# Optimization experiments

Measured on AMD Instinct MI355X. Metric: run time of the kernel, lower is better.

Reference implementation:

```python
import jax, jax.numpy as jnp
import numpy as np

N, E, IN, HID, OUT, H = 10000, 320000, 256, 128, 128, 4
SLOPE = 0.2

def setup_inputs() -> dict:
    key = jax.random.key(0)
    ks = jax.random.split(key, 12)
    s = lambda d: 1.0 / np.sqrt(d)
    return {
        "x": jax.random.normal(ks[0], (N, IN), jnp.float32),
        "edge_index": jax.random.randint(ks[1], (2, E), 0, N, jnp.int32),
        "W1": jax.random.normal(ks[2], (IN, H * HID), jnp.float32) * s(IN),
        "a_src1": jax.random.normal(ks[3], (H, HID), jnp.float32) * s(HID),
        "a_dst1": jax.random.normal(ks[4], (H, HID), jnp.float32) * s(HID),
        "b1": jnp.zeros((H * HID,), jnp.float32),
        "W2": jax.random.normal(ks[5], (H * HID, H * OUT), jnp.float32) * s(H * HID),
        "a_src2": jax.random.normal(ks[6], (H, OUT), jnp.float32) * s(OUT),
        "a_dst2": jax.random.normal(ks[7], (H, OUT), jnp.float32) * s(OUT),
        "b2": jnp.zeros((OUT,), jnp.float32),
    }

def _gat_layer(x, src, dst, W, a_src, a_dst, bias, concat, C):
    n = x.shape[0]
    h = (x @ W).reshape(n, H, C)                      # [N,H,C]
    alpha_s = jnp.einsum('nhc,hc->nh', h, a_src)      # [N,H]
    alpha_d = jnp.einsum('nhc,hc->nh', h, a_dst)
    e = jax.nn.leaky_relu(alpha_s[src] + alpha_d[dst], SLOPE)  # [E,H]
    # segment softmax over incoming edges of each dst node
    m = jax.ops.segment_max(e, dst, num_segments=n)   # [N,H]
    m = jnp.where(jnp.isfinite(m), m, 0.0)
    ex = jnp.exp(e - m[dst])
    denom = jax.ops.segment_sum(ex, dst, num_segments=n)
    alpha = ex / (denom[dst] + 1e-16)                 # [E,H]
    msg = h[src] * alpha[:, :, None]                  # [E,H,C]
    out = jax.ops.segment_sum(msg, dst, num_segments=n)  # [N,H,C]
    out = out.reshape(n, H * C) if concat else out.mean(axis=1)
    return out + bias

def reference(x, edge_index, W1, a_src1, a_dst1, b1, W2, a_src2, a_dst2, b2):
    n = x.shape[0]
    loops = jnp.arange(n, dtype=edge_index.dtype)
    src = jnp.concatenate([edge_index[0], loops])
    dst = jnp.concatenate([edge_index[1], loops])
    h = _gat_layer(x, src, dst, W1, a_src1, a_dst1, b1, True, HID)
    h = jax.nn.relu(h)  # dropout is identity in eval mode
    out = _gat_layer(h, src, dst, W2, a_src2, a_dst2, b2, False, OUT)
    return out
```

## Files before the change

### kernel.cpp

```cpp
#include <hip/hip_runtime.h>
#include <hip/hip_fp16.h>
#include <math.h>

#define Nn 10000
#define Ee 320000
#define EE 330000
#define INF_ 256
#define NH 4
#define OUTC 128
#define F1 512
#define F2 512
#define SLOPE 0.2f
#define STRIDE 80

#define SC_BLOCKS 1290
#define CONVX_BLOCKS 2500
#define TW1_BLOCKS 512
#define TW2_BLOCKS 1024

static __device__ __forceinline__ float lrelu(float x) { return fmaxf(x, SLOPE * x); }

using frag_ab = __attribute__((ext_vector_type(8))) _Float16;
using frag_c  = __attribute__((ext_vector_type(4))) float;

__global__ void prep(const int* __restrict__ ei, int* counts, int* __restrict__ csr,
                     const float* __restrict__ x, const float* __restrict__ W1,
                     const float* __restrict__ W2, _Float16* __restrict__ xh,
                     _Float16* __restrict__ w1t, _Float16* __restrict__ w2t) {
    int b = blockIdx.x, t = threadIdx.x;
    if (b < SC_BLOCKS) {
        int e = b * 256 + t;
        if (e < EE) {
            int src, dst;
            if (e < Ee) { src = ei[e]; dst = ei[Ee + e]; }
            else        { src = e - Ee; dst = e - Ee; }
            int slot = atomicAdd(&counts[dst], 1);
            if (slot < STRIDE) csr[dst * STRIDE + slot] = src;
        }
    } else if (b < SC_BLOCKS + CONVX_BLOCKS) {
        int i = ((b - SC_BLOCKS) * 256 + t) * 4;
        float4 v = *(const float4*)(x + i);
        _Float16 oh[4];
        oh[0] = (_Float16)v.x; oh[1] = (_Float16)v.y;
        oh[2] = (_Float16)v.z; oh[3] = (_Float16)v.w;
        *(float2*)(xh + i) = *(float2*)oh;
    } else if (b < SC_BLOCKS + CONVX_BLOCKS + TW1_BLOCKS) {
        int bb = b - SC_BLOCKS - CONVX_BLOCKS;
        int n = (bb & 7) * 64 + (t & 63);
        int k = (bb >> 3) * 4 + (t >> 6);
        w1t[(size_t)n * INF_ + k] = (_Float16)W1[(size_t)k * F1 + n];
    } else {
        int bb = b - SC_BLOCKS - CONVX_BLOCKS - TW1_BLOCKS;
        int n = (bb & 7) * 64 + (t & 63);
        int k = (bb >> 3) * 4 + (t >> 6);
        w2t[(size_t)n * F1 + k] = (_Float16)W2[(size_t)k * F2 + n];
    }
}

#define LDK 40
__global__ __launch_bounds__(256) void mfma_gemm(const _Float16* __restrict__ A,
                                                 const _Float16* __restrict__ BT,
                                                 _Float16* __restrict__ C,
                                                 const float* __restrict__ a_src,
                                                 const float* __restrict__ a_dst,
                                                 float* __restrict__ as_out,
                                                 float* __restrict__ ad_out,
                                                 int M, int K) {
    __shared__ _Float16 As[64 * LDK];
    __shared__ _Float16 Bs[128 * LDK];
    const int tid = threadIdx.x;
    const int wave = tid >> 6, lane = tid & 63;
    const int q = lane >> 4, ml = lane & 15;
    const int bm = blockIdx.x * 64, bn = blockIdx.y * 128;
    const int head = blockIdx.y;
    const int srow = tid >> 2, scol = (tid & 3) * 8;

    frag_c acc[8];
#pragma unroll
    for (int f = 0; f < 8; f++)
#pragma unroll
        for (int r = 0; r < 4; r++) acc[f][r] = 0.f;

    for (int k0 = 0; k0 < K; k0 += 32) {
        int gm = bm + srow;
        frag_ab av;
        if (gm < M) av = *(const frag_ab*)(A + (size_t)gm * K + k0 + scol);
        else {
#pragma unroll
            for (int j = 0; j < 8; j++) av[j] = (_Float16)0.f;
        }
        *(frag_ab*)&As[srow * LDK + scol] = av;
        *(frag_ab*)&Bs[srow * LDK + scol] =
            *(const frag_ab*)(BT + (size_t)(bn + srow) * K + k0 + scol);
        *(frag_ab*)&Bs[(64 + srow) * LDK + scol] =
            *(const frag_ab*)(BT + (size_t)(bn + 64 + srow) * K + k0 + scol);
        __syncthreads();
        frag_ab a = *(frag_ab*)&As[(wave * 16 + ml) * LDK + q * 8];
#pragma unroll
        for (int f = 0; f < 8; f++) {
            frag_ab b = *(frag_ab*)&Bs[(f * 16 + ml) * LDK + q * 8];
            acc[f] = __builtin_amdgcn_mfma_f32_16x16x32_f16(a, b, acc[f], 0, 0, 0);
        }
        __syncthreads();
    }
    float asum[4] = {}, dsum[4] = {};
#pragma unroll
    for (int f = 0; f < 8; f++) {
        int cl = f * 16 + ml;
        int col = bn + cl;
        float sa = a_src[head * 128 + cl];
        float da = a_dst[head * 128 + cl];
#pragma unroll
        for (int r = 0; r < 4; r++) {
            int row = bm + wave * 16 + q * 4 + r;
            if (row < M) C[(size_t)row * (NH * 128) + col] = (_Float16)acc[f][r];
            asum[r] += acc[f][r] * sa;
            dsum[r] += acc[f][r] * da;
        }
    }
#pragma unroll
    for (int r = 0; r < 4; r++) {
#pragma unroll
        for (int off = 1; off < 16; off <<= 1) {
            asum[r] += __shfl_xor(asum[r], off);
            dsum[r] += __shfl_xor(dsum[r], off);
        }
    }
    if (ml == 0) {
#pragma unroll
        for (int r = 0; r < 4; r++) {
            int row = bm + wave * 16 + q * 4 + r;
            if (row < M) {
                as_out[(size_t)head * M + row] = asum[r];
                ad_out[(size_t)head * M + row] = dsum[r];
            }
        }
    }
}

__global__ __launch_bounds__(256) void passAB1(const int* __restrict__ counts,
                                               const int* __restrict__ csr,
                                               const float* __restrict__ as,
                                               const float* __restrict__ ad,
                                               const _Float16* __restrict__ hh,
                                               const float* __restrict__ b1,
                                               _Float16* __restrict__ agg) {
    __shared__ int2 ew[16][84];
    int head = blockIdx.x & 3;
    int qw = threadIdx.x >> 4;
    int l = threadIdx.x & 15;
    int n = (blockIdx.x >> 2) * 16 + qw;
    int deg = counts[n]; if (deg > STRIDE) deg = STRIDE;
    int pdeg = (deg + 7) & ~7;
    const float* ash = as + (size_t)head * Nn;
    float adh = ad[(size_t)head * Nn + n];
    int base = n * STRIDE;
    float m = -1e30f;
    for (int k = l; k < pdeg; k += 16) {
        int src = 0; float v = -1e30f;
        if (k < deg) {
            src = csr[base + k];
            v = lrelu(ash[src] + adh);
        }
        ew[qw][k] = make_int2(src, __float_as_int(v));
        m = fmaxf(m, v);
    }
    m = fmaxf(m, __shfl_xor(m, 1));
    m = fmaxf(m, __shfl_xor(m, 2));
    m = fmaxf(m, __shfl_xor(m, 4));
    m = fmaxf(m, __shfl_xor(m, 8));
    float s = 0.f;
    for (int k = l; k < pdeg; k += 16) {
        float e = __expf(__int_as_float(ew[qw][k].y) - m);
        ew[qw][k].y = __float_as_int(e);
        s += e;
    }
    s += __shfl_xor(s, 1);
    s += __shfl_xor(s, 2);
    s += __shfl_xor(s, 4);
    s += __shfl_xor(s, 8);
    float inv = 1.f / (s + 1e-16f);
    int c = head * 128 + (l << 3);
    float acc[8] = {};
    for (int kk = 0; kk < pdeg; kk += 8) {
        int2 p[8];
#pragma unroll
        for (int j = 0; j < 8; j++) p[j] = ew[qw][kk + j];
#pragma unroll
        for (int j = 0; j < 8; j++) {
            float w = __int_as_float(p[j].y);
            frag_ab r = *(const frag_ab*)(hh + (size_t)p[j].x * F1 + c);
#pragma unroll
            for (int u = 0; u < 8; u++) acc[u] = fmaf((float)r[u], w, acc[u]);
        }
    }
    _Float16 oh[8];
#pragma unroll
    for (int j = 0; j < 8; j++)
        oh[j] = (_Float16)fmaxf(acc[j] * inv + b1[c + j], 0.f);
    *(float4*)&agg[(size_t)n * F1 + c] = *(float4*)oh;
}

__global__ __launch_bounds__(256) void passAB2(const int* __restrict__ counts,
                                               const int* __restrict__ csr,
                                               const float* __restrict__ as,
                                               const float* __restrict__ ad,
                                               const _Float16* __restrict__ hh,
                                               _Float16* __restrict__ tmp) {
    __shared__ int2 ew[16][84];
    int head = blockIdx.x & 3;
    int qw = threadIdx.x >> 4;
    int l = threadIdx.x & 15;
    int n = (blockIdx.x >> 2) * 16 + qw;
    int deg = counts[n]; if (deg > STRIDE) deg = STRIDE;
    int pdeg = (deg + 7) & ~7;
    const float* ash = as + (size_t)head * Nn;
    float adh = ad[(size_t)head * Nn + n];
    int base = n * STRIDE;
    float m = -1e30f;
    for (int k = l; k < pdeg; k += 16) {
        int src = 0; float v = -1e30f;
        if (k < deg) {
            src = csr[base + k];
            v = lrelu(ash[src] + adh);
        }
        ew[qw][k] = make_int2(src, __float_as_int(v));
        m = fmaxf(m, v);
    }
    m = fmaxf(m, __shfl_xor(m, 1));
    m = fmaxf(m, __shfl_xor(m, 2));
    m = fmaxf(m, __shfl_xor(m, 4));
    m = fmaxf(m, __shfl_xor(m, 8));
    float s = 0.f;
    for (int k = l; k < pdeg; k += 16) {
        float e = __expf(__int_as_float(ew[qw][k].y) - m);
        ew[qw][k].y = __float_as_int(e);
        s += e;
    }
    s += __shfl_xor(s, 1);
    s += __shfl_xor(s, 2);
    s += __shfl_xor(s, 4);
    s += __shfl_xor(s, 8);
    float inv = 1.f / (s + 1e-16f);
    int c = head * 128 + (l << 3);
    float acc[8] = {};
    for (int kk = 0; kk < pdeg; kk += 8) {
        int2 p[8];
#pragma unroll
        for (int j = 0; j < 8; j++) p[j] = ew[qw][kk + j];
#pragma unroll
        for (int j = 0; j < 8; j++) {
            float w = __int_as_float(p[j].y);
            frag_ab r = *(const frag_ab*)(hh + (size_t)p[j].x * F2 + c);
#pragma unroll
            for (int u = 0; u < 8; u++) acc[u] = fmaf((float)r[u], w, acc[u]);
        }
    }
    float qq = 0.25f * inv;
    _Float16 oh[8];
#pragma unroll
    for (int j = 0; j < 8; j++) oh[j] = (_Float16)(acc[j] * qq);
    *(float4*)&tmp[(size_t)n * F2 + c] = *(float4*)oh;
}

__global__ void reduce4(const _Float16* __restrict__ tmp, const float* __restrict__ b2,
                        float* __restrict__ out) {
    int i = blockIdx.x * 256 + threadIdx.x;
    if (i >= Nn * OUTC) return;
    int n = i >> 7, oc = i & 127;
    const _Float16* tp = tmp + (size_t)n * 512 + oc;
    out[i] = (float)tp[0] + (float)tp[128] + (float)tp[256] + (float)tp[384] + b2[oc];
}

extern "C" void kernel_launch(void* const* d_in, const int* in_sizes, int n_in,
                              void* d_out, int out_size, void* d_ws, size_t ws_size,
                              hipStream_t stream) {
    const float* x      = (const float*)d_in[0];
    const int*   ei     = (const int*)d_in[1];
    const float* W1     = (const float*)d_in[2];
    const float* a_src1 = (const float*)d_in[3];
    const float* a_dst1 = (const float*)d_in[4];
    const float* b1     = (const float*)d_in[5];
    const float* W2     = (const float*)d_in[6];
    const float* a_src2 = (const float*)d_in[7];
    const float* a_dst2 = (const float*)d_in[8];
    const float* b2     = (const float*)d_in[9];
    float* out = (float*)d_out;

    const size_t NF = (size_t)Nn * F1;
    float* f = (float*)d_ws;
    _Float16* tmp = (_Float16*)f;
    float* as1   = f + NF;
    float* ad1   = as1 + Nn;
    float* as1h  = as1;
    float* ad1h  = as1 + (size_t)NH * Nn;
    float* as2h  = ad1h + (size_t)NH * Nn;
    float* ad2h  = as2h + (size_t)NH * Nn;
    (void)ad1;
    int* csr     = (int*)(ad2h + (size_t)NH * Nn);
    _Float16* hh   = (_Float16*)(csr + (size_t)Nn * STRIDE);
    _Float16* aggh = hh + NF;
    _Float16* xh   = aggh + NF;
    _Float16* w1t  = xh + (size_t)Nn * INF_;
    _Float16* w2t  = w1t + (size_t)F1 * INF_;
    int* counts    = (int*)(w2t + (size_t)F2 * F1);

    (void)hipMemsetAsync(counts, 0, Nn * sizeof(int), stream);
    prep<<<SC_BLOCKS + CONVX_BLOCKS + TW1_BLOCKS + TW2_BLOCKS, 256, 0, stream>>>(
        ei, counts, csr, x, W1, W2, xh, w1t, w2t);

    mfma_gemm<<<dim3((Nn + 63) / 64, F1 / 128), 256, 0, stream>>>(
        xh, w1t, hh, a_src1, a_dst1, as1h, ad1h, Nn, INF_);
    passAB1<<<(Nn / 16) * 4, 256, 0, stream>>>(counts, csr, as1h, ad1h, hh, b1, aggh);

    mfma_gemm<<<dim3((Nn + 63) / 64, F2 / 128), 256, 0, stream>>>(
        aggh, w2t, hh, a_src2, a_dst2, as2h, ad2h, Nn, F1);
    passAB2<<<(Nn / 16) * 4, 256, 0, stream>>>(counts, csr, as2h, ad2h, hh, tmp);
    reduce4<<<(Nn * OUTC + 255) / 256, 256, 0, stream>>>(tmp, b2, out);
}
```

Baseline: 188.3 us.

## Fuse GAT pipeline into persistent megakernel with grid-wide atomic barriers

```diff
diff --git a/kernel.cpp b/kernel.cpp
--- a/kernel.cpp
+++ b/kernel.cpp
@@ -12,67 +12,77 @@
 #define F2 512
 #define SLOPE 0.2f
 #define STRIDE 80
-
-#define SC_BLOCKS 1290
-#define CONVX_BLOCKS 2500
-#define TW1_BLOCKS 512
-#define TW2_BLOCKS 1024
+#define LDK 40
+#define NT 256
+#define GRID 1024
+#define GT (GRID * NT)
+#define MT 157
+#define GEMM_TILES (MT * NH)
+#define PASS_VB ((Nn / 16) * NH)
 
 static __device__ __forceinline__ float lrelu(float x) { return fmaxf(x, SLOPE * x); }
 
 using frag_ab = __attribute__((ext_vector_type(8))) _Float16;
 using frag_c  = __attribute__((ext_vector_type(4))) float;
 
-__global__ void prep(const int* __restrict__ ei, int* counts, int* __restrict__ csr,
-                     const float* __restrict__ x, const float* __restrict__ W1,
-                     const float* __restrict__ W2, _Float16* __restrict__ xh,
-                     _Float16* __restrict__ w1t, _Float16* __restrict__ w2t) {
-    int b = blockIdx.x, t = threadIdx.x;
-    if (b < SC_BLOCKS) {
-        int e = b * 256 + t;
-        if (e < EE) {
-            int src, dst;
-            if (e < Ee) { src = ei[e]; dst = ei[Ee + e]; }
-            else        { src = e - Ee; dst = e - Ee; }
-            int slot = atomicAdd(&counts[dst], 1);
-            if (slot < STRIDE) csr[dst * STRIDE + slot] = src;
-        }
-    } else if (b < SC_BLOCKS + CONVX_BLOCKS) {
-        int i = ((b - SC_BLOCKS) * 256 + t) * 4;
-        float4 v = *(const float4*)(x + i);
-        _Float16 oh[4];
-        oh[0] = (_Float16)v.x; oh[1] = (_Float16)v.y;
-        oh[2] = (_Float16)v.z; oh[3] = (_Float16)v.w;
-        *(float2*)(xh + i) = *(float2*)oh;
-    } else if (b < SC_BLOCKS + CONVX_BLOCKS + TW1_BLOCKS) {
-        int bb = b - SC_BLOCKS - CONVX_BLOCKS;
-        int n = (bb & 7) * 64 + (t & 63);
-        int k = (bb >> 3) * 4 + (t >> 6);
-        w1t[(size_t)n * INF_ + k] = (_Float16)W1[(size_t)k * F1 + n];
-    } else {
-        int bb = b - SC_BLOCKS - CONVX_BLOCKS - TW1_BLOCKS;
-        int n = (bb & 7) * 64 + (t & 63);
-        int k = (bb >> 3) * 4 + (t >> 6);
-        w2t[(size_t)n * F1 + k] = (_Float16)W2[(size_t)k * F2 + n];
-    }
-}
-
-#define LDK 40
-__global__ __launch_bounds__(256) void mfma_gemm(const _Float16* __restrict__ A,
-                                                 const _Float16* __restrict__ BT,
-                                                 _Float16* __restrict__ C,
-                                                 const float* __restrict__ a_src,
-                                                 const float* __restrict__ a_dst,
-                                                 float* __restrict__ as_out,
-                                                 float* __restrict__ ad_out,
-                                                 int M, int K) {
-    __shared__ _Float16 As[64 * LDK];
-    __shared__ _Float16 Bs[128 * LDK];
+struct Params {
+    const float* x; const int* ei;
+    const float* W1; const float* a_src1; const float* a_dst1; const float* b1;
+    const float* W2; const float* a_src2; const float* a_dst2; const float* b2;
+    float* out;
+    int* counts; int* csr; int* bar;
+    _Float16* hh; _Float16* aggh; _Float16* w1t; _Float16* w2t; _Float16* tmp;
+    float* as1; float* ad1; float* as2; float* ad2;
+};
+
+static __device__ __forceinline__ void gbar(int* bar, int ph) {
+    __syncthreads();
+    if (threadIdx.x == 0) {
+        __hip_atomic_fetch_add(&bar[ph], 1, __ATOMIC_ACQ_REL, __HIP_MEMORY_SCOPE_AGENT);
+        while (__hip_atomic_load(&bar[ph], __ATOMIC_ACQUIRE, __HIP_MEMORY_SCOPE_AGENT) < GRID)
+            __builtin_amdgcn_s_sleep(1);
+    }
+    __syncthreads();
+}
+
+static __device__ void prep0(const Params& p) {
+    int gt = blockIdx.x * NT + threadIdx.x;
+    for (int i = gt; i < Nn; i += GT) p.counts[i] = 0;
+    for (int i = gt; i < F1 * INF_; i += GT) {
+        int n = i >> 8, k = i & 255;
+        p.w1t[i] = (_Float16)p.W1[(size_t)k * F1 + n];
+    }
+    for (int i = gt; i < F2 * F1; i += GT) {
+        int n = i >> 9, k = i & 511;
+        p.w2t[i] = (_Float16)p.W2[(size_t)k * F2 + n];
+    }
+}
+
+static __device__ void scatter_edges(const Params& p, int bi, int nb) {
+    for (int e = bi * NT + threadIdx.x; e < EE; e += nb * NT) {
+        int src, dst;
+        if (e < Ee) { src = p.ei[e]; dst = p.ei[Ee + e]; }
+        else        { src = e - Ee; dst = e - Ee; }
+        int slot = atomicAdd(&p.counts[dst], 1);
+        if (slot < STRIDE) p.csr[dst * STRIDE + slot] = src;
+    }
+}
+
+template <bool AF32>
+static __device__ void gemm_tile(const _Float16* __restrict__ Ah,
+                                 const float* __restrict__ Af,
+                                 const _Float16* __restrict__ BT,
+                                 _Float16* __restrict__ C,
+                                 const float* __restrict__ a_src,
+                                 const float* __restrict__ a_dst,
+                                 float* __restrict__ as_out,
+                                 float* __restrict__ ad_out,
+                                 int K, int bmi, int head,
+                                 _Float16* As, _Float16* Bs) {
     const int tid = threadIdx.x;
     const int wave = tid >> 6, lane = tid & 63;
     const int q = lane >> 4, ml = lane & 15;
-    const int bm = blockIdx.x * 64, bn = blockIdx.y * 128;
-    const int head = blockIdx.y;
+    const int bm = bmi * 64, bn = head * 128;
     const int srow = tid >> 2, scol = (tid & 3) * 8;
 
     frag_c acc[8];
@@ -84,8 +94,19 @@
     for (int k0 = 0; k0 < K; k0 += 32) {
         int gm = bm + srow;
         frag_ab av;
-        if (gm < M) av = *(const frag_ab*)(A + (size_t)gm * K + k0 + scol);
-        else {
+        if (gm < Nn) {
+            if constexpr (AF32) {
+                const float* Ap = Af + (size_t)gm * K + k0 + scol;
+                float4 v0 = *(const float4*)Ap;
+                float4 v1 = *(const float4*)(Ap + 4);
+                av[0] = (_Float16)v0.x; av[1] = (_Float16)v0.y;
+                av[2] = (_Float16)v0.z; av[3] = (_Float16)v0.w;
+                av[4] = (_Float16)v1.x; av[5] = (_Float16)v1.y;
+                av[6] = (_Float16)v1.z; av[7] = (_Float16)v1.w;
+            } else {
+                av = *(const frag_ab*)(Ah + (size_t)gm * K + k0 + scol);
+            }
+        } else {
 #pragma unroll
             for (int j = 0; j < 8; j++) av[j] = (_Float16)0.f;
         }
@@ -113,7 +134,7 @@
 #pragma unroll
         for (int r = 0; r < 4; r++) {
             int row = bm + wave * 16 + q * 4 + r;
-            if (row < M) C[(size_t)row * (NH * 128) + col] = (_Float16)acc[f][r];
+            if (row < Nn) C[(size_t)row * (NH * 128) + col] = (_Float16)acc[f][r];
             asum[r] += acc[f][r] * sa;
             dsum[r] += acc[f][r] * da;
         }
@@ -130,26 +151,26 @@
 #pragma unroll
         for (int r = 0; r < 4; r++) {
             int row = bm + wave * 16 + q * 4 + r;
-            if (row < M) {
-                as_out[(size_t)head * M + row] = asum[r];
-                ad_out[(size_t)head * M + row] = dsum[r];
+            if (row < Nn) {
+                as_out[(size_t)head * Nn + row] = asum[r];
+                ad_out[(size_t)head * Nn + row] = dsum[r];
             }
         }
     }
 }
 
-__global__ __launch_bounds__(256) void passAB1(const int* __restrict__ counts,
-                                               const int* __restrict__ csr,
-                                               const float* __restrict__ as,
-                                               const float* __restrict__ ad,
-                                               const _Float16* __restrict__ hh,
-                                               const float* __restrict__ b1,
-                                               _Float16* __restrict__ agg) {
-    __shared__ int2 ew[16][84];
-    int head = blockIdx.x & 3;
+template <int LAYER>
+static __device__ void pass_body(int vb, const int* __restrict__ counts,
+                                 const int* __restrict__ csr,
+                                 const float* __restrict__ as,
+                                 const float* __restrict__ ad,
+                                 const _Float16* __restrict__ hh,
+                                 const float* __restrict__ b1,
+                                 _Float16* __restrict__ outp, int2 (*ew)[84]) {
+    int head = vb & 3;
     int qw = threadIdx.x >> 4;
     int l = threadIdx.x & 15;
-    int n = (blockIdx.x >> 2) * 16 + qw;
+    int n = (vb >> 2) * 16 + qw;
     int deg = counts[n]; if (deg > STRIDE) deg = STRIDE;
     int pdeg = (deg + 7) & ~7;
     const float* ash = as + (size_t)head * Nn;
@@ -183,138 +204,146 @@
     int c = head * 128 + (l << 3);
     float acc[8] = {};
     for (int kk = 0; kk < pdeg; kk += 8) {
-        int2 p[8];
-#pragma unroll
-        for (int j = 0; j < 8; j++) p[j] = ew[qw][kk + j];
+        int2 pj[8];
+#pragma unroll
+        for (int j = 0; j < 8; j++) pj[j] = ew[qw][kk + j];
 #pragma unroll
         for (int j = 0; j < 8; j++) {
-            float w = __int_as_float(p[j].y);
-            frag_ab r = *(const frag_ab*)(hh + (size_t)p[j].x * F1 + c);
+            float w = __int_as_float(pj[j].y);
+            frag_ab r = *(const frag_ab*)(hh + (size_t)pj[j].x * 512 + c);
 #pragma unroll
             for (int u = 0; u < 8; u++) acc[u] = fmaf((float)r[u], w, acc[u]);
         }
     }
     _Float16 oh[8];
-#pragma unroll
-    for (int j = 0; j < 8; j++)
-        oh[j] = (_Float16)fmaxf(acc[j] * inv + b1[c + j], 0.f);
-    *(float4*)&agg[(size_t)n * F1 + c] = *(float4*)oh;
-}
-
-__global__ __launch_bounds__(256) void passAB2(const int* __restrict__ counts,
-                                               const int* __restrict__ csr,
-                                               const float* __restrict__ as,
-                                               const float* __restrict__ ad,
-                                               const _Float16* __restrict__ hh,
-                                               _Float16* __restrict__ tmp) {
+    if constexpr (LAYER == 1) {
+#pragma unroll
+        for (int j = 0; j < 8; j++)
+            oh[j] = (_Float16)fmaxf(acc[j] * inv + b1[c + j], 0.f);
+    } else {
+        float qq = 0.25f * inv;
+#pragma unroll
+        for (int j = 0; j < 8; j++) oh[j] = (_Float16)(acc[j] * qq);
+    }
+    *(float4*)&outp[(size_t)n * 512 + c] = *(float4*)oh;
+}
+
+static __device__ void reduce_out(const Params& p) {
+    int gt = blockIdx.x * NT + threadIdx.x;
+    for (int i = gt; i < Nn * OUTC; i += GT) {
+        int n = i >> 7, oc = i & 127;
+        const _Float16* tp = p.tmp + (size_t)n * 512 + oc;
+        p.out[i] = (float)tp[0] + (float)tp[128] + (float)tp[256] + (float)tp[384] + p.b2[oc];
+    }
+}
+
+__global__ __launch_bounds__(NT, 4) void mega(Params p) {
+    __shared__ _Float16 As[64 * LDK];
+    __shared__ _Float16 Bs[128 * LDK];
     __shared__ int2 ew[16][84];
-    int head = blockIdx.x & 3;
-    int qw = threadIdx.x >> 4;
-    int l = threadIdx.x & 15;
-    int n = (blockIdx.x >> 2) * 16 + qw;
-    int deg = counts[n]; if (deg > STRIDE) deg = STRIDE;
-    int pdeg = (deg + 7) & ~7;
-    const float* ash = as + (size_t)head * Nn;
-    float adh = ad[(size_t)head * Nn + n];
-    int base = n * STRIDE;
-    float m = -1e30f;
-    for (int k = l; k < pdeg; k += 16) {
-        int src = 0; float v = -1e30f;
-        if (k < deg) {
-            src = csr[base + k];
-            v = lrelu(ash[src] + adh);
-        }
-        ew[qw][k] = make_int2(src, __float_as_int(v));
-        m = fmaxf(m, v);
-    }
-    m = fmaxf(m, __shfl_xor(m, 1));
-    m = fmaxf(m, __shfl_xor(m, 2));
-    m = fmaxf(m, __shfl_xor(m, 4));
-    m = fmaxf(m, __shfl_xor(m, 8));
-    float s = 0.f;
-    for (int k = l; k < pdeg; k += 16) {
-        float e = __expf(__int_as_float(ew[qw][k].y) - m);
-        ew[qw][k].y = __float_as_int(e);
-        s += e;
-    }
-    s += __shfl_xor(s, 1);
-    s += __shfl_xor(s, 2);
-    s += __shfl_xor(s, 4);
-    s += __shfl_xor(s, 8);
-    float inv = 1.f / (s + 1e-16f);
-    int c = head * 128 + (l << 3);
-    float acc[8] = {};
-    for (int kk = 0; kk < pdeg; kk += 8) {
-        int2 p[8];
-#pragma unroll
-        for (int j = 0; j < 8; j++) p[j] = ew[qw][kk + j];
-#pragma unroll
-        for (int j = 0; j < 8; j++) {
-            float w = __int_as_float(p[j].y);
-            frag_ab r = *(const frag_ab*)(hh + (size_t)p[j].x * F2 + c);
-#pragma unroll
-            for (int u = 0; u < 8; u++) acc[u] = fmaf((float)r[u], w, acc[u]);
-        }
-    }
-    float qq = 0.25f * inv;
-    _Float16 oh[8];
-#pragma unroll
-    for (int j = 0; j < 8; j++) oh[j] = (_Float16)(acc[j] * qq);
-    *(float4*)&tmp[(size_t)n * F2 + c] = *(float4*)oh;
-}
-
-__global__ void reduce4(const _Float16* __restrict__ tmp, const float* __restrict__ b2,
-                        float* __restrict__ out) {
-    int i = blockIdx.x * 256 + threadIdx.x;
-    if (i >= Nn * OUTC) return;
-    int n = i >> 7, oc = i & 127;
-    const _Float16* tp = tmp + (size_t)n * 512 + oc;
-    out[i] = (float)tp[0] + (float)tp[128] + (float)tp[256] + (float)tp[384] + b2[oc];
-}
+
+    prep0(p);
+    gbar(p.bar, 0);
+
+    if (blockIdx.x < GEMM_TILES)
+        gemm_tile<true>(nullptr, p.x, p.w1t, p.hh, p.a_src1, p.a_dst1, p.as1, p.ad1,
+                        INF_, blockIdx.x % MT, blockIdx.x / MT, As, Bs);
+    else
+        scatter_edges(p, blockIdx.x - GEMM_TILES, GRID - GEMM_TILES);
+    gbar(p.bar, 1);
+
+    for (int vb = blockIdx.x; vb < PASS_VB; vb += GRID)
+        pass_body<1>(vb, p.counts, p.csr, p.as1, p.ad1, p.hh, p.b1, p.aggh, ew);
+    gbar(p.bar, 2);
+
+    if (blockIdx.x < GEMM_TILES)
+        gemm_tile<false>(p.aggh, nullptr, p.w2t, p.hh, p.a_src2, p.a_dst2, p.as2, p.ad2,
+                         F1, blockIdx.x % MT, blockIdx.x / MT, As, Bs);
+    gbar(p.bar, 3);
+
+    for (int vb = blockIdx.x; vb < PASS_VB; vb += GRID)
+        pass_body<2>(vb, p.counts, p.csr, p.as2, p.ad2, p.hh, nullptr, p.tmp, ew);
+    gbar(p.bar, 4);
+
+    reduce_out(p);
+}
+
+__global__ __launch_bounds__(NT) void k_p0(Params p) { prep0(p); }
+__global__ __launch_bounds__(NT) void k_p1(Params p) {
+    __shared__ _Float16 As[64 * LDK];
+    __shared__ _Float16 Bs[128 * LDK];
+    if (blockIdx.x < GEMM_TILES)
+        gemm_tile<true>(nullptr, p.x, p.w1t, p.hh, p.a_src1, p.a_dst1, p.as1, p.ad1,
+                        INF_, blockIdx.x % MT, blockIdx.x / MT, As, Bs);
+    else
+        scatter_edges(p, blockIdx.x - GEMM_TILES, GRID - GEMM_TILES);
+}
+__global__ __launch_bounds__(NT) void k_p2(Params p) {
+    __shared__ int2 ew[16][84];
+    for (int vb = blockIdx.x; vb < PASS_VB; vb += GRID)
+        pass_body<1>(vb, p.counts, p.csr, p.as1, p.ad1, p.hh, p.b1, p.aggh, ew);
+}
+__global__ __launch_bounds__(NT) void k_p3(Params p) {
+    __shared__ _Float16 As[64 * LDK];
+    __shared__ _Float16 Bs[128 * LDK];
+    if (blockIdx.x < GEMM_TILES)
+        gemm_tile<false>(p.aggh, nullptr, p.w2t, p.hh, p.a_src2, p.a_dst2, p.as2, p.ad2,
+                         F1, blockIdx.x % MT, blockIdx.x / MT, As, Bs);
+}
+__global__ __launch_bounds__(NT) void k_p4(Params p) {
+    __shared__ int2 ew[16][84];
+    for (int vb = blockIdx.x; vb < PASS_VB; vb += GRID)
+        pass_body<2>(vb, p.counts, p.csr, p.as2, p.ad2, p.hh, nullptr, p.tmp, ew);
+}
+__global__ __launch_bounds__(NT) void k_p5(Params p) { reduce_out(p); }
 
 extern "C" void kernel_launch(void* const* d_in, const int* in_sizes, int n_in,
                               void* d_out, int out_size, void* d_ws, size_t ws_size,
                               hipStream_t stream) {
-    const float* x      = (const float*)d_in[0];
-    const int*   ei     = (const int*)d_in[1];
-    const float* W1     = (const float*)d_in[2];
-    const float* a_src1 = (const float*)d_in[3];
-    const float* a_dst1 = (const float*)d_in[4];
-    const float* b1     = (const float*)d_in[5];
-    const float* W2     = (const float*)d_in[6];
-    const float* a_src2 = (const float*)d_in[7];
-    const float* a_dst2 = (const float*)d_in[8];
-    const float* b2     = (const float*)d_in[9];
-    float* out = (float*)d_out;
-
-    const size_t NF = (size_t)Nn * F1;
-    float* f = (float*)d_ws;
-    _Float16* tmp = (_Float16*)f;
-    float* as1   = f + NF;
-    float* ad1   = as1 + Nn;
-    float* as1h  = as1;
-    float* ad1h  = as1 + (size_t)NH * Nn;
-    float* as2h  = ad1h + (size_t)NH * Nn;
-    float* ad2h  = as2h + (size_t)NH * Nn;
-    (void)ad1;
-    int* csr     = (int*)(ad2h + (size_t)NH * Nn);
-    _Float16* hh   = (_Float16*)(csr + (size_t)Nn * STRIDE);
-    _Float16* aggh = hh + NF;
-    _Float16* xh   = aggh + NF;
-    _Float16* w1t  = xh + (size_t)Nn * INF_;
-    _Float16* w2t  = w1t + (size_t)F1 * INF_;
-    int* counts    = (int*)(w2t + (size_t)F2 * F1);
-
-    (void)hipMemsetAsync(counts, 0, Nn * sizeof(int), stream);
-    prep<<<SC_BLOCKS + CONVX_BLOCKS + TW1_BLOCKS + TW2_BLOCKS, 256, 0, stream>>>(
-        ei, counts, csr, x, W1, W2, xh, w1t, w2t);
-
-    mfma_gemm<<<dim3((Nn + 63) / 64, F1 / 128), 256, 0, stream>>>(
-        xh, w1t, hh, a_src1, a_dst1, as1h, ad1h, Nn, INF_);
-    passAB1<<<(Nn / 16) * 4, 256, 0, stream>>>(counts, csr, as1h, ad1h, hh, b1, aggh);
-
-    mfma_gemm<<<dim3((Nn + 63) / 64, F2 / 128), 256, 0, stream>>>(
-        aggh, w2t, hh, a_src2, a_dst2, as2h, ad2h, Nn, F1);
-    passAB2<<<(Nn / 16) * 4, 256, 0, stream>>>(counts, csr, as2h, ad2h, hh, tmp);
-    reduce4<<<(Nn * OUTC + 255) / 256, 256, 0, stream>>>(tmp, b2, out);
-}
+    Params p;
+    p.x      = (const float*)d_in[0];
+    p.ei     = (const int*)d_in[1];
+    p.W1     = (const float*)d_in[2];
+    p.a_src1 = (const float*)d_in[3];
+    p.a_dst1 = (const float*)d_in[4];
+    p.b1     = (const float*)d_in[5];
+    p.W2     = (const float*)d_in[6];
+    p.a_src2 = (const float*)d_in[7];
+    p.a_dst2 = (const float*)d_in[8];
+    p.b2     = (const float*)d_in[9];
+    p.out    = (float*)d_out;
+
+    char* w = (char*)d_ws;
+    p.tmp  = (_Float16*)w; w += (size_t)Nn * F2 * 2;
+    p.hh   = (_Float16*)w; w += (size_t)Nn * F1 * 2;
+    p.aggh = (_Float16*)w; w += (size_t)Nn * F1 * 2;
+    p.w1t  = (_Float16*)w; w += (size_t)F1 * INF_ * 2;
+    p.w2t  = (_Float16*)w; w += (size_t)F2 * F1 * 2;
+    p.as1  = (float*)w;    w += (size_t)NH * Nn * 4;
+    p.ad1  = (float*)w;    w += (size_t)NH * Nn * 4;
+    p.as2  = (float*)w;    w += (size_t)NH * Nn * 4;
+    p.ad2  = (float*)w;    w += (size_t)NH * Nn * 4;
+    p.csr  = (int*)w;      w += (size_t)Nn * STRIDE * 4;
+    p.counts = (int*)w;    w += (size_t)Nn * 4;
+    p.bar  = (int*)w;      w += 8 * 4;
+
+    static int occ = -1;
+    if (occ < 0) {
+        int nb = 0;
+        if (hipOccupancyMaxActiveBlocksPerMultiprocessor(&nb, mega, NT, 0) != hipSuccess)
+            nb = 0;
+        occ = nb;
+    }
+
+    if (occ >= 4) {
+        (void)hipMemsetAsync(p.bar, 0, 8 * sizeof(int), stream);
+        mega<<<GRID, NT, 0, stream>>>(p);
+    } else {
+        k_p0<<<GRID, NT, 0, stream>>>(p);
+        k_p1<<<GRID, NT, 0, stream>>>(p);
+        k_p2<<<GRID, NT, 0, stream>>>(p);
+        k_p3<<<GEMM_TILES, NT, 0, stream>>>(p);
+        k_p4<<<GRID, NT, 0, stream>>>(p);
+        k_p5<<<GRID, NT, 0, stream>>>(p);
+    }
+}
```

Result: slower. 198.0 us (+5.1%).

## Fuse x fp16 conversion into GEMM1, fuse head-mean into layer-2 aggregation

Applied to the files above, without the earlier changes.

```diff
diff --git a/kernel.cpp b/kernel.cpp
--- a/kernel.cpp
+++ b/kernel.cpp
@@ -12,11 +12,13 @@
 #define F2 512
 #define SLOPE 0.2f
 #define STRIDE 80
+#define LDK 40
+#define MT 157
 
 #define SC_BLOCKS 1290
-#define CONVX_BLOCKS 2500
 #define TW1_BLOCKS 512
 #define TW2_BLOCKS 1024
+#define GEMM_GRID 640
 
 static __device__ __forceinline__ float lrelu(float x) { return fmaxf(x, SLOPE * x); }
 
@@ -24,8 +26,7 @@
 using frag_c  = __attribute__((ext_vector_type(4))) float;
 
 __global__ void prep(const int* __restrict__ ei, int* counts, int* __restrict__ csr,
-                     const float* __restrict__ x, const float* __restrict__ W1,
-                     const float* __restrict__ W2, _Float16* __restrict__ xh,
+                     const float* __restrict__ W1, const float* __restrict__ W2,
                      _Float16* __restrict__ w1t, _Float16* __restrict__ w2t) {
     int b = blockIdx.x, t = threadIdx.x;
     if (b < SC_BLOCKS) {
@@ -37,42 +38,34 @@
             int slot = atomicAdd(&counts[dst], 1);
             if (slot < STRIDE) csr[dst * STRIDE + slot] = src;
         }
-    } else if (b < SC_BLOCKS + CONVX_BLOCKS) {
-        int i = ((b - SC_BLOCKS) * 256 + t) * 4;
-        float4 v = *(const float4*)(x + i);
-        _Float16 oh[4];
-        oh[0] = (_Float16)v.x; oh[1] = (_Float16)v.y;
-        oh[2] = (_Float16)v.z; oh[3] = (_Float16)v.w;
-        *(float2*)(xh + i) = *(float2*)oh;
-    } else if (b < SC_BLOCKS + CONVX_BLOCKS + TW1_BLOCKS) {
-        int bb = b - SC_BLOCKS - CONVX_BLOCKS;
+    } else if (b < SC_BLOCKS + TW1_BLOCKS) {
+        int bb = b - SC_BLOCKS;
         int n = (bb & 7) * 64 + (t & 63);
         int k = (bb >> 3) * 4 + (t >> 6);
         w1t[(size_t)n * INF_ + k] = (_Float16)W1[(size_t)k * F1 + n];
     } else {
-        int bb = b - SC_BLOCKS - CONVX_BLOCKS - TW1_BLOCKS;
+        int bb = b - SC_BLOCKS - TW1_BLOCKS;
         int n = (bb & 7) * 64 + (t & 63);
         int k = (bb >> 3) * 4 + (t >> 6);
         w2t[(size_t)n * F1 + k] = (_Float16)W2[(size_t)k * F2 + n];
     }
 }
 
-#define LDK 40
-__global__ __launch_bounds__(256) void mfma_gemm(const _Float16* __restrict__ A,
-                                                 const _Float16* __restrict__ BT,
-                                                 _Float16* __restrict__ C,
-                                                 const float* __restrict__ a_src,
-                                                 const float* __restrict__ a_dst,
-                                                 float* __restrict__ as_out,
-                                                 float* __restrict__ ad_out,
-                                                 int M, int K) {
-    __shared__ _Float16 As[64 * LDK];
-    __shared__ _Float16 Bs[128 * LDK];
+template <bool AF32>
+static __device__ void gemm_tile(const _Float16* __restrict__ Ah,
+                                 const float* __restrict__ Af,
+                                 const _Float16* __restrict__ BT,
+                                 _Float16* __restrict__ C,
+                                 const float* __restrict__ a_src,
+                                 const float* __restrict__ a_dst,
+                                 float* __restrict__ as_out,
+                                 float* __restrict__ ad_out,
+                                 int K, int bmi, int head,
+                                 _Float16* As, _Float16* Bs) {
     const int tid = threadIdx.x;
     const int wave = tid >> 6, lane = tid & 63;
     const int q = lane >> 4, ml = lane & 15;
-    const int bm = blockIdx.x * 64, bn = blockIdx.y * 128;
-    const int head = blockIdx.y;
+    const int bm = bmi * 64, bn = head * 128;
     const int srow = tid >> 2, scol = (tid & 3) * 8;
 
     frag_c acc[8];
@@ -84,8 +77,19 @@
     for (int k0 = 0; k0 < K; k0 += 32) {
         int gm = bm + srow;
         frag_ab av;
-        if (gm < M) av = *(const frag_ab*)(A + (size_t)gm * K + k0 + scol);
-        else {
+        if (gm < Nn) {
+            if constexpr (AF32) {
+                const float* Ap = Af + (size_t)gm * K + k0 + scol;
+                float4 v0 = *(const float4*)Ap;
+                float4 v1 = *(const float4*)(Ap + 4);
+                av[0] = (_Float16)v0.x; av[1] = (_Float16)v0.y;
+                av[2] = (_Float16)v0.z; av[3] = (_Float16)v0.w;
+                av[4] = (_Float16)v1.x; av[5] = (_Float16)v1.y;
+                av[6] = (_Float16)v1.z; av[7] = (_Float16)v1.w;
+            } else {
+                av = *(const frag_ab*)(Ah + (size_t)gm * K + k0 + scol);
+            }
+        } else {
 #pragma unroll
             for (int j = 0; j < 8; j++) av[j] = (_Float16)0.f;
         }
@@ -113,7 +117,7 @@
 #pragma unroll
         for (int r = 0; r < 4; r++) {
             int row = bm + wave * 16 + q * 4 + r;
-            if (row < M) C[(size_t)row * (NH * 128) + col] = (_Float16)acc[f][r];
+            if (row < Nn) C[(size_t)row * (NH * 128) + col] = (_Float16)acc[f][r];
             asum[r] += acc[f][r] * sa;
             dsum[r] += acc[f][r] * da;
         }
@@ -130,12 +134,46 @@
 #pragma unroll
         for (int r = 0; r < 4; r++) {
             int row = bm + wave * 16 + q * 4 + r;
-            if (row < M) {
-                as_out[(size_t)head * M + row] = asum[r];
-                ad_out[(size_t)head * M + row] = dsum[r];
+            if (row < Nn) {
+                as_out[(size_t)head * Nn + row] = asum[r];
+                ad_out[(size_t)head * Nn + row] = dsum[r];
             }
         }
     }
+}
+
+__global__ __launch_bounds__(256) void gemm1(const float* __restrict__ x,
+                                             const _Float16* __restrict__ w1t,
+                                             _Float16* __restrict__ hh,
+                                             const float* __restrict__ a_src,
+                                             const float* __restrict__ a_dst,
+                                             float* __restrict__ as_out,
+                                             float* __restrict__ ad_out) {
+    __shared__ _Float16 As[64 * LDK];
+    __shared__ _Float16 Bs[128 * LDK];
+    int bid = blockIdx.x;
+    int m8 = bid & 7, rest = bid >> 3;
+    int h = rest & 3, mhi = rest >> 2;
+    int m = mhi * 8 + m8;
+    if (m >= MT) return;
+    gemm_tile<true>(nullptr, x, w1t, hh, a_src, a_dst, as_out, ad_out, INF_, m, h, As, Bs);
+}
+
+__global__ __launch_bounds__(256) void gemm2(const _Float16* __restrict__ aggh,
+                                             const _Float16* __restrict__ w2t,
+                                             _Float16* __restrict__ hh,
+                                             const float* __restrict__ a_src,
+                                             const float* __restrict__ a_dst,
+                                             float* __restrict__ as_out,
+                                             float* __restrict__ ad_out) {
+    __shared__ _Float16 As[64 * LDK];
+    __shared__ _Float16 Bs[128 * LDK];
+    int bid = blockIdx.x;
+    int m8 = bid & 7, rest = bid >> 3;
+    int h = rest & 3, mhi = rest >> 2;
+    int m = mhi * 8 + m8;
+    if (m >= MT) return;
+    gemm_tile<false>(aggh, nullptr, w2t, hh, a_src, a_dst, as_out, ad_out, F1, m, h, As, Bs);
 }
 
 __global__ __launch_bounds__(256) void passAB1(const int* __restrict__ counts,
@@ -183,13 +221,13 @@
     int c = head * 128 + (l << 3);
     float acc[8] = {};
     for (int kk = 0; kk < pdeg; kk += 8) {
-        int2 p[8];
-#pragma unroll
-        for (int j = 0; j < 8; j++) p[j] = ew[qw][kk + j];
+        int2 pj[8];
+#pragma unroll
+        for (int j = 0; j < 8; j++) pj[j] = ew[qw][kk + j];
 #pragma unroll
         for (int j = 0; j < 8; j++) {
-            float w = __int_as_float(p[j].y);
-            frag_ab r = *(const frag_ab*)(hh + (size_t)p[j].x * F1 + c);
+            float w = __int_as_float(pj[j].y);
+            frag_ab r = *(const frag_ab*)(hh + (size_t)pj[j].x * F1 + c);
 #pragma unroll
             for (int u = 0; u < 8; u++) acc[u] = fmaf((float)r[u], w, acc[u]);
         }
@@ -201,30 +239,33 @@
     *(float4*)&agg[(size_t)n * F1 + c] = *(float4*)oh;
 }
 
-__global__ __launch_bounds__(256) void passAB2(const int* __restrict__ counts,
-                                               const int* __restrict__ csr,
-                                               const float* __restrict__ as,
-                                               const float* __restrict__ ad,
-                                               const _Float16* __restrict__ hh,
-                                               _Float16* __restrict__ tmp) {
-    __shared__ int2 ew[16][84];
-    int head = blockIdx.x & 3;
-    int qw = threadIdx.x >> 4;
-    int l = threadIdx.x & 15;
-    int n = (blockIdx.x >> 2) * 16 + qw;
+__global__ __launch_bounds__(256) void passC(const int* __restrict__ counts,
+                                             const int* __restrict__ csr,
+                                             const float* __restrict__ as,
+                                             const float* __restrict__ ad,
+                                             const _Float16* __restrict__ hh,
+                                             const float* __restrict__ b2,
+                                             float* __restrict__ out) {
+    __shared__ int   esrc[4][80];
+    __shared__ float ewgt[4][4][80];
+    int w = threadIdx.x >> 6;
+    int lane = threadIdx.x & 63;
+    int h = lane >> 4, i = lane & 15;
+    int n = blockIdx.x * 4 + w;
     int deg = counts[n]; if (deg > STRIDE) deg = STRIDE;
     int pdeg = (deg + 7) & ~7;
-    const float* ash = as + (size_t)head * Nn;
-    float adh = ad[(size_t)head * Nn + n];
+    float adh = ad[(size_t)h * Nn + n];
+    const float* ash = as + (size_t)h * Nn;
     int base = n * STRIDE;
     float m = -1e30f;
-    for (int k = l; k < pdeg; k += 16) {
+    for (int k = i; k < pdeg; k += 16) {
         int src = 0; float v = -1e30f;
         if (k < deg) {
             src = csr[base + k];
             v = lrelu(ash[src] + adh);
         }
-        ew[qw][k] = make_int2(src, __float_as_int(v));
+        if (h == 0) esrc[w][k] = src;
+        ewgt[w][h][k] = v;
         m = fmaxf(m, v);
     }
     m = fmaxf(m, __shfl_xor(m, 1));
@@ -232,44 +273,42 @@
     m = fmaxf(m, __shfl_xor(m, 4));
     m = fmaxf(m, __shfl_xor(m, 8));
     float s = 0.f;
-    for (int k = l; k < pdeg; k += 16) {
-        float e = __expf(__int_as_float(ew[qw][k].y) - m);
-        ew[qw][k].y = __float_as_int(e);
+    for (int k = i; k < pdeg; k += 16) {
+        float e = __expf(ewgt[w][h][k] - m);
+        ewgt[w][h][k] = e;
         s += e;
     }
     s += __shfl_xor(s, 1);
     s += __shfl_xor(s, 2);
     s += __shfl_xor(s, 4);
     s += __shfl_xor(s, 8);
-    float inv = 1.f / (s + 1e-16f);
-    int c = head * 128 + (l << 3);
+    float scale = 0.25f / (s + 1e-16f);
+    int c = lane << 3;
     float acc[8] = {};
     for (int kk = 0; kk < pdeg; kk += 8) {
-        int2 p[8];
-#pragma unroll
-        for (int j = 0; j < 8; j++) p[j] = ew[qw][kk + j];
+        int s8[8]; float w8[8];
+#pragma unroll
+        for (int j = 0; j < 8; j++) { s8[j] = esrc[w][kk + j]; w8[j] = ewgt[w][h][kk + j]; }
 #pragma unroll
         for (int j = 0; j < 8; j++) {
-            float w = __int_as_float(p[j].y);
-            frag_ab r = *(const frag_ab*)(hh + (size_t)p[j].x * F2 + c);
-#pragma unroll
-            for (int u = 0; u < 8; u++) acc[u] = fmaf((float)r[u], w, acc[u]);
-        }
-    }
-    float qq = 0.25f * inv;
-    _Float16 oh[8];
-#pragma unroll
-    for (int j = 0; j < 8; j++) oh[j] = (_Float16)(acc[j] * qq);
-    *(float4*)&tmp[(size_t)n * F2 + c] = *(float4*)oh;
-}
-
-__global__ void reduce4(const _Float16* __restrict__ tmp, const float* __restrict__ b2,
-                        float* __restrict__ out) {
-    int i = blockIdx.x * 256 + threadIdx.x;
-    if (i >= Nn * OUTC) return;
-    int n = i >> 7, oc = i & 127;
-    const _Float16* tp = tmp + (size_t)n * 512 + oc;
-    out[i] = (float)tp[0] + (float)tp[128] + (float)tp[256] + (float)tp[384] + b2[oc];
+            frag_ab r = *(const frag_ab*)(hh + (size_t)s8[j] * F2 + c);
+#pragma unroll
+            for (int u = 0; u < 8; u++) acc[u] = fmaf((float)r[u], w8[j], acc[u]);
+        }
+    }
+#pragma unroll
+    for (int u = 0; u < 8; u++) {
+        acc[u] *= scale;
+        acc[u] += __shfl_xor(acc[u], 16);
+        acc[u] += __shfl_xor(acc[u], 32);
+    }
+    if (h == 0) {
+        float o[8];
+#pragma unroll
+        for (int j = 0; j < 8; j++) o[j] = acc[j] + b2[(i << 3) + j];
+        *(float4*)&out[(size_t)n * OUTC + (i << 3)]     = *(float4*)&o[0];
+        *(float4*)&out[(size_t)n * OUTC + (i << 3) + 4] = *(float4*)&o[4];
+    }
 }
 
 extern "C" void kernel_launch(void* const* d_in, const int* in_sizes, int n_in,
@@ -287,34 +326,25 @@
     const float* b2     = (const float*)d_in[9];
     float* out = (float*)d_out;
 
-    const size_t NF = (size_t)Nn * F1;
-    float* f = (float*)d_ws;
-    _Float16* tmp = (_Float16*)f;
-    float* as1   = f + NF;
-    float* ad1   = as1 + Nn;
-    float* as1h  = as1;
-    float* ad1h  = as1 + (size_t)NH * Nn;
-    float* as2h  = ad1h + (size_t)NH * Nn;
-    float* ad2h  = as2h + (size_t)NH * Nn;
-    (void)ad1;
-    int* csr     = (int*)(ad2h + (size_t)NH * Nn);
-    _Float16* hh   = (_Float16*)(csr + (size_t)Nn * STRIDE);
-    _Float16* aggh = hh + NF;
-    _Float16* xh   = aggh + NF;
-    _Float16* w1t  = xh + (size_t)Nn * INF_;
-    _Float16* w2t  = w1t + (size_t)F1 * INF_;
-    int* counts    = (int*)(w2t + (size_t)F2 * F1);
+    char* w = (char*)d_ws;
+    _Float16* hh   = (_Float16*)w; w += (size_t)Nn * F1 * 2;
+    _Float16* aggh = (_Float16*)w; w += (size_t)Nn * F1 * 2;
+    _Float16* w1t  = (_Float16*)w; w += (size_t)F1 * INF_ * 2;
+    _Float16* w2t  = (_Float16*)w; w += (size_t)F2 * F1 * 2;
+    float* as1     = (float*)w;    w += (size_t)NH * Nn * 4;
+    float* ad1     = (float*)w;    w += (size_t)NH * Nn * 4;
+    float* as2     = (float*)w;    w += (size_t)NH * Nn * 4;
+    float* ad2     = (float*)w;    w += (size_t)NH * Nn * 4;
+    int* csr       = (int*)w;      w += (size_t)Nn * STRIDE * 4;
+    int* counts    = (int*)w;      w += (size_t)Nn * 4;
 
     (void)hipMemsetAsync(counts, 0, Nn * sizeof(int), stream);
-    prep<<<SC_BLOCKS + CONVX_BLOCKS + TW1_BLOCKS + TW2_BLOCKS, 256, 0, stream>>>(
-        ei, counts, csr, x, W1, W2, xh, w1t, w2t);
-
-    mfma_gemm<<<dim3((Nn + 63) / 64, F1 / 128), 256, 0, stream>>>(
-        xh, w1t, hh, a_src1, a_dst1, as1h, ad1h, Nn, INF_);
-    passAB1<<<(Nn / 16) * 4, 256, 0, stream>>>(counts, csr, as1h, ad1h, hh, b1, aggh);
-
-    mfma_gemm<<<dim3((Nn + 63) / 64, F2 / 128), 256, 0, stream>>>(
-        aggh, w2t, hh, a_src2, a_dst2, as2h, ad2h, Nn, F1);
-    passAB2<<<(Nn / 16) * 4, 256, 0, stream>>>(counts, csr, as2h, ad2h, hh, tmp);
-    reduce4<<<(Nn * OUTC + 255) / 256, 256, 0, stream>>>(tmp, b2, out);
-}
+    prep<<<SC_BLOCKS + TW1_BLOCKS + TW2_BLOCKS, 256, 0, stream>>>(
+        ei, counts, csr, W1, W2, w1t, w2t);
+
+    gemm1<<<GEMM_GRID, 256, 0, stream>>>(x, w1t, hh, a_src1, a_dst1, as1, ad1);
+    passAB1<<<(Nn / 16) * NH, 256, 0, stream>>>(counts, csr, as1, ad1, hh, b1, aggh);
+
+    gemm2<<<GEMM_GRID, 256, 0, stream>>>(aggh, w2t, hh, a_src2, a_dst2, as2, ad2);
+    passC<<<Nn / 4, 256, 0, stream>>>(counts, csr, as2, ad2, hh, b2, out);
+}
```

After: 199.7 us. 1.06x slower.
